# Kernel optimization log

Measured on AMD Instinct MI355X. Metric: run time of the kernel, lower is better.

## Reference

```python
import jax, jax.numpy as jnp
import numpy as np

K = 20      # kNN neighbors
H = 4       # attention heads
EPS = 1e-5  # BatchNorm eps
NEG = 0.2   # LeakyReLU negative slope


def lrelu(x):
    return jnp.where(x >= 0, x, NEG * x)


def bn(x, g, b):
    # eval-mode BatchNorm: running_mean=0, running_var=1
    return x * (g / jnp.sqrt(1.0 + EPS)) + b


def knn_idx(x):
    # x: (B, N, C) -> (B, N, K) indices of K nearest neighbors (incl. self)
    inner = -2.0 * jnp.einsum('bnc,bmc->bnm', x, x)
    xx = jnp.sum(x * x, axis=-1)
    pd = -xx[:, :, None] - inner - xx[:, None, :]  # negative squared distance
    return jax.lax.top_k(pd, K)[1]


def edge_conv(x, w, g, b):
    # EdgeConv: gather kNN features, cat(nbr-ctr, ctr), 1x1 conv, BN, LeakyReLU, max over K
    idx = knn_idx(x)                                   # (B,N,K)
    nbr = jax.vmap(lambda f, i: f[i])(x, idx)          # (B,N,K,C)
    ctr = jnp.broadcast_to(x[:, :, None, :], nbr.shape)
    e = jnp.concatenate([nbr - ctr, ctr], axis=-1)     # (B,N,K,2C)
    h = lrelu(bn(jnp.einsum('bnkc,oc->bnko', e, w), g, b))
    return jnp.max(h, axis=2)                          # (B,N,Cout)


def mha(x, w_in, b_in, w_out, b_out):
    # Faithful to source: (B,N,E) fed to nn.MultiheadAttention with batch_first=False,
    # so seq length L=B and batch=N (attention mixes across the batch axis).
    L, Nb, E = x.shape
    d = E // H
    qkv = x @ w_in.T + b_in
    q, k, v = jnp.split(qkv, 3, axis=-1)
    q = q.reshape(L, Nb, H, d) * (1.0 / np.sqrt(d))
    k = k.reshape(L, Nb, H, d)
    v = v.reshape(L, Nb, H, d)
    a = jax.nn.softmax(jnp.einsum('lnhd,mnhd->nhlm', q, k), axis=-1)
    o = jnp.einsum('nhlm,mnhd->lnhd', a, v).reshape(L, Nb, E)
    return o @ w_out.T + b_out


def setup_inputs():
    ks = iter(jax.random.split(jax.random.key(0), 64))
    def rn(shape, s=0.05):
        return jax.random.normal(next(ks), shape, jnp.float32) * s
    def gamma(c):
        return 1.0 + rn((c,), 0.1)
    B, N = 8, 1024
    inp = {'x': rn((B, N, 3), 1.0)}
    for i, (ci, co) in enumerate([(6, 64), (128, 64), (128, 128), (256, 256)], 1):
        inp[f'w{i}'] = rn((co, ci)); inp[f'g{i}'] = gamma(co); inp[f'b{i}'] = rn((co,))
    for i, e in enumerate([64, 64, 128, 256], 1):
        inp[f'a{i}_wi'] = rn((3 * e, e)); inp[f'a{i}_bi'] = rn((3 * e,))
        inp[f'a{i}_wo'] = rn((e, e));     inp[f'a{i}_bo'] = rn((e,))
    inp['w5'] = rn((1024, 512)); inp['g5'] = gamma(1024); inp['b5'] = rn((1024,))
    inp['l1w'] = rn((512, 2048)); inp['g6'] = gamma(512); inp['b6'] = rn((512,))
    inp['l2w'] = rn((256, 512)); inp['l2b'] = rn((256,))
    inp['g7'] = gamma(256); inp['b7'] = rn((256,))
    inp['l3w'] = rn((40, 256)); inp['l3b'] = rn((40,))
    return inp


def reference(x, w1, g1, b1, a1_wi, a1_bi, a1_wo, a1_bo,
              w2, g2, b2, a2_wi, a2_bi, a2_wo, a2_bo,
              w3, g3, b3, a3_wi, a3_bi, a3_wo, a3_bo,
              w4, g4, b4, a4_wi, a4_bi, a4_wo, a4_bo,
              w5, g5, b5, l1w, g6, b6, l2w, l2b, g7, b7, l3w, l3b):
    x1 = edge_conv(x, w1, g1, b1)
    x1 = mha(x1, a1_wi, a1_bi, a1_wo, a1_bo) + x1
    x2 = edge_conv(x1, w2, g2, b2)
    x2 = mha(x2, a2_wi, a2_bi, a2_wo, a2_bo) + x2
    x3 = edge_conv(x2, w3, g3, b3)
    x3 = mha(x3, a3_wi, a3_bi, a3_wo, a3_bo) + x3
    x4 = edge_conv(x3, w4, g4, b4)
    x4 = mha(x4, a4_wi, a4_bi, a4_wo, a4_bo) + x4
    h = lrelu(bn(jnp.concatenate([x1, x2, x3, x4], axis=-1) @ w5.T, g5, b5))  # (B,N,1024)
    feat = jnp.concatenate([jnp.max(h, axis=1), jnp.mean(h, axis=1)], axis=-1)  # (B,2048)
    h = lrelu(bn(feat @ l1w.T, g6, b6))
    h = lrelu(bn(h @ l2w.T + l2b, g7, b7))  # dropout is eval-mode identity
    return h @ l3w.T + l3b  # (B, 40)
```

## Files before the change

### kernel.cpp

```cpp
#include <hip/hip_runtime.h>
#include <hip/hip_bf16.h>

#define B_ 8
#define N_ 1024
#define K_ 20
#define BN_ (B_*N_)

#define BN_SCALE 0.9999950000374997f

typedef __attribute__((ext_vector_type(8))) short short8;
typedef __attribute__((ext_vector_type(4))) float f32x4;

__device__ __forceinline__ float US2F(unsigned short u) {
    union { unsigned u; float f; } c; c.u = ((unsigned)u) << 16; return c.f;
}
__device__ __forceinline__ unsigned short F2BF(float f) {
    union { float f; unsigned u; } c; c.f = f;
    unsigned r = c.u + 0x7FFF + ((c.u >> 16) & 1);
    return (unsigned short)(r >> 16);
}

__device__ __forceinline__ void ldsld16(const unsigned short* g, unsigned short* l) {
    __builtin_amdgcn_global_load_lds(
        (const __attribute__((address_space(1))) void*)g,
        (__attribute__((address_space(3))) void*)l, 16, 0, 0);
}

struct DetP { const unsigned short* g[7]; };
__device__ __forceinline__ int det_isbf(const DetP& dp) {
    int cnt = 0;
    #pragma unroll
    for (int i = 0; i < 7; i++) {
        float v = US2F(dp.g[i][0]);
        if (v > 0.5f && v < 1.5f) cnt++;
    }
    return cnt >= 4;
}

struct TPar { const void* src; void* dst; int O, I, blk0, mode; };
struct TList { TPar p[44]; };
struct TrP { const void* src; float* dst; int O, I, bx, blk0; };

__global__ __launch_bounds__(256) void k_prep(TList tl, int nent,
                                              TrP q0, TrP q1, TrP q2,
                                              int nbp, int nbtr,
                                              const void* x0, DetP dp,
                                              unsigned short* __restrict__ xa,
                                              unsigned short* __restrict__ xb,
                                              float* __restrict__ xx1) {
    __shared__ int sbf;
    if (threadIdx.x == 0) sbf = det_isbf(dp);
    __syncthreads();
    const int isbf = sbf;
    auto ld0 = [&](int idx) {
        return isbf ? US2F(((const unsigned short*)x0)[idx])
                    : ((const float*)x0)[idx];
    };
    const int bid = blockIdx.x;
    if (bid >= nbp + nbtr) {
        int blk = bid - nbp - nbtr;
        if (blk >= (BN_ * 32) / 256) {
            int i = (blk - (BN_ * 32) / 256) * 256 + threadIdx.x;
            if (i >= BN_) return;
            float s = 0.f;
            #pragma unroll
            for (int c = 0; c < 3; c++) { float v = ld0(i * 3 + c); s += v * v; }
            xx1[i] = s;
            return;
        }
        const int e = blk * 256 + threadIdx.x;
        const int i = e >> 5, p = e & 31;
        unsigned short va = 0, vb = 0;
        if (p < 9) {
            const int seg = p / 3, c = p - seg * 3;
            const float v = ld0(i * 3 + c);
            const unsigned short h = F2BF(v);
            const unsigned short l = F2BF(v - US2F(h));
            va = (seg == 1) ? l : h;
            vb = (seg < 2) ? h : l;
        }
        xa[e] = va; xb[e] = vb;
        return;
    }
    if (bid >= nbp) {
        int blk = bid - nbp;
        TrP p = q0;
        if (blk >= q2.blk0) p = q2; else if (blk >= q1.blk0) p = q1;
        blk -= p.blk0;
        const int tx = threadIdx.x & 31, ty = threadIdx.x >> 5;
        const int bi = blk % p.bx, bo = blk / p.bx;
        const int i0 = bi * 32, o0 = bo * 32;
        __shared__ float s[32][33];
        #pragma unroll
        for (int r = 0; r < 4; r++) {
            const int o = o0 + ty + r * 8, i = i0 + tx;
            if (o < p.O && i < p.I) {
                const size_t e = (size_t)o * p.I + i;
                s[ty + r * 8][tx] = isbf ? US2F(((const unsigned short*)p.src)[e])
                                         : ((const float*)p.src)[e];
            }
        }
        __syncthreads();
        #pragma unroll
        for (int r = 0; r < 4; r++) {
            const int i = i0 + ty + r * 8, o = o0 + tx;
            if (i < p.I && o < p.O) p.dst[(size_t)i * p.O + o] = s[tx][ty + r * 8];
        }
        return;
    }
    int blk = bid;
    int wi = 0;
    for (int j = nent - 1; j >= 0; j--) { if (blk >= tl.p[j].blk0) { wi = j; break; } }
    const TPar p = tl.p[wi];
    int e = (blk - p.blk0) * 256 + threadIdx.x;
    int n = p.O * p.I;
    if (e >= n) return;
    if (p.mode == 4) { ((float*)p.dst)[e] = 0.f; return; }
    int o = e / p.I, i = e - o * p.I;
    float v = isbf ? US2F(((const unsigned short*)p.src)[e])
                   : ((const float*)p.src)[e];
    if (p.mode == 0) {
        ((float*)p.dst)[(size_t)i * p.O + o] = v;
    } else if (p.mode == 2) {
        ((unsigned short*)p.dst)[e] = F2BF(v);
    } else {
        const int C = p.I >> 1;
        if (i < C) ((unsigned short*)p.dst)[(size_t)o * C + i] = F2BF(v);
        else       ((unsigned short*)p.dst)[(size_t)(p.O + o) * C + (i - C)] = F2BF(v);
    }
}

template<int KP, int TM, int TN>
__device__ __forceinline__ void pdm_dev(int bid,
                                        const unsigned short* __restrict__ xa,
                                        const unsigned short* __restrict__ xb,
                                        const float* __restrict__ xx,
                                        float* __restrict__ pd) {
    const int b = bid & 7;
    const int tt = bid >> 3;
    const int rb = (tt >> 3) * TM, cb = (tt & 7) * TN;
    const unsigned short* Ab = xa + (size_t)b * N_ * KP;
    const unsigned short* Bb = xb + (size_t)b * N_ * KP;
    const float* xxb = xx + (size_t)b * N_;
    const int t = threadIdx.x;
    __shared__ __align__(16) unsigned short As[2][TM * 32];
    __shared__ __align__(16) unsigned short Bs[2][TN * 32];
    const int w = t >> 6, lane = t & 63;
    constexpr int QR = TM / 2, QC = TN / 2;
    constexpr int MR = QR / 16, NR = QC / 16;
    const int wr = (w & 1) * QR, wc = (w >> 1) * QC;
    const int fr = lane & 15, q = lane >> 4;
    f32x4 acc[MR][NR] = {};

    auto STAGE = [&](int buf, int k0) {
        constexpr int AT = TM * 4;
        #pragma unroll
        for (int R = 0; R < (AT + 255) / 256; R++) {
            const int G = t + R * 256;
            if (AT >= (R + 1) * 256 || G < AT) {
                const int m = G >> 2, gs = (G & 3) ^ ((m >> 1) & 3);
                ldsld16(&Ab[(size_t)(rb + m) * KP + k0 + gs * 8], &As[buf][w * 512 + R * 2048]);
            }
        }
        constexpr int BT = TN * 4;
        #pragma unroll
        for (int R = 0; R < (BT + 255) / 256; R++) {
            const int G = t + R * 256;
            if (BT >= (R + 1) * 256 || G < BT) {
                const int n = G >> 2, gs = (G & 3) ^ ((n >> 1) & 3);
                ldsld16(&Bb[(size_t)(cb + n) * KP + k0 + gs * 8], &Bs[buf][w * 512 + R * 2048]);
            }
        }
    };

    constexpr int NT = KP / 32;
    STAGE(0, 0);
    asm volatile("s_waitcnt vmcnt(0)" ::: "memory");
    __builtin_amdgcn_s_barrier();
    int cur = 0;
    for (int ts = 0; ts < NT; ++ts) {
        if (ts + 1 < NT) STAGE(cur ^ 1, (ts + 1) * 32);
        short8 af[MR], bfr[NR];
        #pragma unroll
        for (int mi = 0; mi < MR; mi++) {
            const int r = wr + mi * 16 + fr;
            af[mi] = *reinterpret_cast<const short8*>(&As[cur][r * 32 + ((q ^ ((r >> 1) & 3)) << 3)]);
        }
        #pragma unroll
        for (int ni = 0; ni < NR; ni++) {
            const int r = wc + ni * 16 + fr;
            bfr[ni] = *reinterpret_cast<const short8*>(&Bs[cur][r * 32 + ((q ^ ((r >> 1) & 3)) << 3)]);
        }
        #pragma unroll
        for (int mi = 0; mi < MR; mi++) {
            #pragma unroll
            for (int ni = 0; ni < NR; ni++)
                acc[mi][ni] = __builtin_amdgcn_mfma_f32_16x16x32_bf16(af[mi], bfr[ni], acc[mi][ni], 0, 0, 0);
        }
        asm volatile("s_waitcnt vmcnt(0)" ::: "memory");
        __builtin_amdgcn_s_barrier();
        cur ^= 1;
    }
    float* pdb = pd + (size_t)b * N_ * N_;
    const int cr = (lane >> 4) * 4, cc = lane & 15;
    #pragma unroll
    for (int mi = 0; mi < MR; mi++) {
        #pragma unroll
        for (int ni = 0; ni < NR; ni++) {
            #pragma unroll
            for (int r = 0; r < 4; r++) {
                const int row = rb + wr + mi * 16 + cr + r;
                const int col = cb + wc + ni * 16 + cc;
                pdb[(size_t)row * N_ + col] = 2.f * acc[mi][ni][r] - xxb[col];
            }
        }
    }
}

template<int KD, int NC, int TM, int TN, bool CATA, bool POOL, int SPLIT>
__device__ __forceinline__ void gemm_dev(int bx, int by,
                                         const unsigned short* __restrict__ A,
                                         const unsigned short* __restrict__ A2,
                                         const unsigned short* __restrict__ A3,
                                         const unsigned short* __restrict__ A4,
                                         const unsigned short* __restrict__ Bw,
                                         const float* __restrict__ bias,
                                         const float* __restrict__ resid,
                                         float* __restrict__ Cout,
                                         float* __restrict__ Cz, int yco,
                                         int scale_cols, float qs,
                                         const float* __restrict__ gamma,
                                         const float* __restrict__ beta,
                                         unsigned short* __restrict__ obf,
                                         unsigned* __restrict__ pmaxu,
                                         float* __restrict__ psum,
                                         unsigned short* __restrict__ sxa,
                                         unsigned short* __restrict__ sxb,
                                         float* __restrict__ xxo) {
    const int t = threadIdx.x;
    const int rb = bx * TM, cb = by * TN;
    const int w = t >> 6, lane = t & 63;
    constexpr int QR = TM / 2, QC = TN / 2;
    constexpr int MR = QR / 16, NR = QC / 16;
    const int wr = (w & 1) * QR, wc = (w >> 1) * QC;
    const int fr = lane & 15, q = lane >> 4, fq = q * 8;
    f32x4 acc[MR][NR] = {};
    if constexpr (KD % 32 == 0) {
        __shared__ __align__(16) unsigned short As[2][TM * 32];
        __shared__ __align__(16) unsigned short Bs[2][TN * 32];
        auto STAGE = [&](int buf, int k0) {
            const unsigned short* Asrc = A; int AC = KD, ac0 = k0;
            if constexpr (CATA) {
                if (k0 >= 256)      { Asrc = A4; AC = 256; ac0 = k0 - 256; }
                else if (k0 >= 128) { Asrc = A3; AC = 128; ac0 = k0 - 128; }
                else if (k0 >= 64)  { Asrc = A2; AC = 64;  ac0 = k0 - 64; }
                else                { Asrc = A;  AC = 64;  ac0 = k0; }
            }
            constexpr int AT = TM * 4;
            #pragma unroll
            for (int R = 0; R < (AT + 255) / 256; R++) {
                const int G = t + R * 256;
                if (AT >= (R + 1) * 256 || G < AT) {
                    const int m = G >> 2, gs = (G & 3) ^ ((m >> 1) & 3);
                    ldsld16(&Asrc[(size_t)(rb + m) * AC + ac0 + gs * 8], &As[buf][w * 512 + R * 2048]);
                }
            }
            constexpr int BT = TN * 4;
            #pragma unroll
            for (int R = 0; R < (BT + 255) / 256; R++) {
                const int G = t + R * 256;
                if (BT >= (R + 1) * 256 || G < BT) {
                    const int n = G >> 2, gs = (G & 3) ^ ((n >> 1) & 3);
                    ldsld16(&Bw[(size_t)(cb + n) * KD + k0 + gs * 8], &Bs[buf][w * 512 + R * 2048]);
                }
            }
        };
        constexpr int NT = KD / 32;
        STAGE(0, 0);
        asm volatile("s_waitcnt vmcnt(0)" ::: "memory");
        __builtin_amdgcn_s_barrier();
        int cur = 0;
        for (int ts = 0; ts < NT; ++ts) {
            if (ts + 1 < NT) STAGE(cur ^ 1, (ts + 1) * 32);
            short8 af[MR], bfr[NR];
            #pragma unroll
            for (int mi = 0; mi < MR; mi++) {
                const int r = wr + mi * 16 + fr;
                af[mi] = *reinterpret_cast<const short8*>(&As[cur][r * 32 + ((q ^ ((r >> 1) & 3)) << 3)]);
            }
            #pragma unroll
            for (int ni = 0; ni < NR; ni++) {
                const int r = wc + ni * 16 + fr;
                bfr[ni] = *reinterpret_cast<const short8*>(&Bs[cur][r * 32 + ((q ^ ((r >> 1) & 3)) << 3)]);
            }
            #pragma unroll
            for (int mi = 0; mi < MR; mi++) {
                #pragma unroll
                for (int ni = 0; ni < NR; ni++)
                    acc[mi][ni] = __builtin_amdgcn_mfma_f32_16x16x32_bf16(af[mi], bfr[ni], acc[mi][ni], 0, 0, 0);
            }
            asm volatile("s_waitcnt vmcnt(0)" ::: "memory");
            __builtin_amdgcn_s_barrier();
            cur ^= 1;
        }
    } else {
        __shared__ __align__(16) unsigned short As[TM * 40];
        __shared__ __align__(16) unsigned short Bs[TN * 40];
        for (int k0 = 0; k0 < KD; k0 += 32) {
            __syncthreads();
            #pragma unroll
            for (int u = t; u < TM * 4; u += 256) {
                const int m = u >> 2, c = (u & 3) * 8;
                #pragma unroll
                for (int j = 0; j < 8; j++) {
                    const int kk = k0 + c + j;
                    As[m * 40 + c + j] = (kk < KD) ? A[(size_t)(rb + m) * KD + kk] : (unsigned short)0;
                }
            }
            #pragma unroll
            for (int u = t; u < TN * 4; u += 256) {
                const int n = u >> 2, c = (u & 3) * 8;
                const int gn = cb + n;
                if (gn < NC) {
                    #pragma unroll
                    for (int j = 0; j < 8; j++) {
                        const int kk = k0 + c + j;
                        Bs[n * 40 + c + j] = (kk < KD) ? Bw[(size_t)gn * KD + kk] : (unsigned short)0;
                    }
                } else {
                    short8 z = {};
                    *reinterpret_cast<short8*>(&Bs[n * 40 + c]) = z;
                }
            }
            __syncthreads();
            short8 af[MR], bfr[NR];
            #pragma unroll
            for (int mi = 0; mi < MR; mi++)
                af[mi] = *reinterpret_cast<const short8*>(&As[(wr + mi * 16 + fr) * 40 + fq]);
            #pragma unroll
            for (int ni = 0; ni < NR; ni++)
                bfr[ni] = *reinterpret_cast<const short8*>(&Bs[(wc + ni * 16 + fr) * 40 + fq]);
            #pragma unroll
            for (int mi = 0; mi < MR; mi++) {
                #pragma unroll
                for (int ni = 0; ni < NR; ni++)
                    acc[mi][ni] = __builtin_amdgcn_mfma_f32_16x16x32_bf16(af[mi], bfr[ni], acc[mi][ni], 0, 0, 0);
            }
        }
    }
    const int cr = (lane >> 4) * 4, cc = lane & 15;
    if constexpr (POOL) {
        const int bidx = rb >> 10;
        #pragma unroll
        for (int ni = 0; ni < NR; ni++) {
            const int col = cb + wc + ni * 16 + cc;
            const float gm = gamma[col] * BN_SCALE, bt = beta[col];
            float sm = 0.f, mxv = -3e38f;
            #pragma unroll
            for (int mi = 0; mi < MR; mi++) {
                #pragma unroll
                for (int r = 0; r < 4; r++) {
                    float v = acc[mi][ni][r] * gm + bt;
                    v = v >= 0.f ? v : 0.2f * v;
                    sm += v; mxv = fmaxf(mxv, v);
                }
            }
            sm += __shfl_xor(sm, 16, 64);
            sm += __shfl_xor(sm, 32, 64);
            mxv = fmaxf(mxv, __shfl_xor(mxv, 16, 64));
            mxv = fmaxf(mxv, __shfl_xor(mxv, 32, 64));
            if (lane < 16) {
                atomicAdd(&psum[bidx * 1024 + col], sm);
                unsigned tb = __float_as_uint(mxv);
                tb = (tb & 0x80000000u) ? ~tb : (tb | 0x80000000u);
                atomicMax(&pmaxu[bidx * 1024 + col], tb);
            }
        }
    } else {
        float sx[MR][4] = {};
        #pragma unroll
        for (int mi = 0; mi < MR; mi++) {
            #pragma unroll
            for (int ni = 0; ni < NR; ni++) {
                #pragma unroll
                for (int r = 0; r < 4; r++) {
                    const int row = rb + wr + mi * 16 + cr + r;
                    const int col = cb + wc + ni * 16 + cc;
                    if (col < NC) {
                        float v = acc[mi][ni][r] + (bias ? bias[col] : 0.f);
                        if (col < scale_cols) v *= qs;
                        if (resid) v += resid[(size_t)row * NC + col];
                        if (gamma) {
                            v = v * (gamma[col] * BN_SCALE) + beta[col];
                            v = v >= 0.f ? v : 0.2f * v;
                        }
                        if (yco > 0) {
                            if (col < yco) Cout[(size_t)row * yco + col] = v;
                            else           Cz[(size_t)row * yco + (col - yco)] = v;
                        } else {
                            Cout[(size_t)row * NC + col] = v;
                        }
                        if (obf) obf[(size_t)row * NC + col] = F2BF(v);
                        if constexpr (SPLIT > 0) {
                            constexpr int KP2 = 3 * SPLIT;
                            const unsigned short h = F2BF(v);
                            const unsigned short l = F2BF(v - US2F(h));
                            sxa[(size_t)row * KP2 + 0 * SPLIT + col] = h;
                            sxa[(size_t)row * KP2 + 1 * SPLIT + col] = l;
                            sxa[(size_t)row * KP2 + 2 * SPLIT + col] = h;
                            sxb[(size_t)row * KP2 + 0 * SPLIT + col] = h;
                            sxb[(size_t)row * KP2 + 1 * SPLIT + col] = h;
                            sxb[(size_t)row * KP2 + 2 * SPLIT + col] = l;
                            sx[mi][r] += v * v;
                        }
                    }
                }
            }
        }
        if constexpr (SPLIT > 0) {
            #pragma unroll
            for (int mi = 0; mi < MR; mi++) {
                #pragma unroll
                for (int r = 0; r < 4; r++) {
                    float s = sx[mi][r];
                    s += __shfl_xor(s, 1, 64);
                    s += __shfl_xor(s, 2, 64);
                    s += __shfl_xor(s, 4, 64);
                    s += __shfl_xor(s, 8, 64);
                    if ((lane & 15) == 0)
                        atomicAdd(&xxo[rb + wr + mi * 16 + cr + r], s);
                }
            }
        }
    }
}

template<int KD, int NC, int TM, int TN, bool CATA = false, bool POOL = false, int SPLIT = 0, bool AFF = false>
__global__ __launch_bounds__(256) void k_gemmb(const unsigned short* __restrict__ A,
                                               const unsigned short* __restrict__ A2,
                                               const unsigned short* __restrict__ A3,
                                               const unsigned short* __restrict__ A4,
                                               const unsigned short* __restrict__ Bw,
                                               const float* __restrict__ bias,
                                               const float* __restrict__ resid,
                                               float* __restrict__ Cout,
                                               int scale_cols, float qs,
                                               const float* __restrict__ gamma,
                                               const float* __restrict__ beta,
                                               unsigned short* __restrict__ obf,
                                               unsigned* __restrict__ pmaxu,
                                               float* __restrict__ psum,
                                               unsigned short* __restrict__ sxa,
                                               unsigned short* __restrict__ sxb,
                                               float* __restrict__ xxo) {
    int bx = blockIdx.x;
    if constexpr (AFF) bx = (bx & 7) * (gridDim.x >> 3) + (bx >> 3);
    gemm_dev<KD, NC, TM, TN, CATA, POOL, SPLIT>(bx, blockIdx.y,
        A, A2, A3, A4, Bw, bias, resid, Cout, nullptr, 0, scale_cols, qs, gamma, beta,
        obf, pmaxu, psum, sxa, sxb, xxo);
}

template<int KP, int KDY, int NCY, int TMY, int TNY>
__global__ __launch_bounds__(256) void k_pdmyz(const unsigned short* __restrict__ xa,
                                               const unsigned short* __restrict__ xb,
                                               const float* __restrict__ xx,
                                               float* __restrict__ pd,
                                               const unsigned short* __restrict__ Ay,
                                               const unsigned short* __restrict__ Bwy,
                                               float* __restrict__ Cy,
                                               float* __restrict__ Cz, int yco, int gxy) {
    if ((int)blockIdx.x < 512) { pdm_dev<KP, 128, 128>(blockIdx.x, xa, xb, xx, pd); return; }
    const int g = blockIdx.x - 512;
    const int batch = g & 7, rem = g >> 3;
    const int rpb = gxy >> 3;
    const int bx = batch * rpb + rem % rpb;
    const int by = rem / rpb;
    gemm_dev<KDY, NCY, TMY, TNY, false, false, 0>(bx, by,
        Ay, nullptr, nullptr, nullptr, Bwy, nullptr, nullptr, Cy, Cz, yco, 0, 1.f,
        nullptr, nullptr, nullptr, nullptr, nullptr, nullptr, nullptr, nullptr);
}

template<int CO>
__global__ __launch_bounds__(256) void k_seledge(const float* __restrict__ pd,
                                                 const float* __restrict__ y,
                                                 const float* __restrict__ z,
                                                 const float* __restrict__ g,
                                                 const float* __restrict__ bb,
                                                 float* __restrict__ out,
                                                 unsigned short* __restrict__ outb) {
    const int t = threadIdx.x;
    const int w = t >> 6, lane = t & 63;
    const int blk = blockIdx.x;
    const int b = blk & 7;
    const int i0 = (b << 10) + ((blk >> 3) << 2);
    const int bbase = b << 10;
    __shared__ int sidx[4][K_];
    {
        const int i = i0 + w;
        const float* row = pd + (size_t)b * N_ * N_ + (size_t)(i & 1023) * N_;
        unsigned key[16];
        #pragma unroll
        for (int q = 0; q < 16; q++) {
            const int j = q * 64 + lane;
            unsigned bits = __float_as_uint(row[j]);
            bits = (bits & 0x80000000u) ? ~bits : (bits | 0x80000000u);
            key[q] = (bits & 0xFFFFFC00u) | (unsigned)(N_ - 1 - j);
        }
        int myj = 0;
        for (int kk = 0; kk < K_; kk++) {
            unsigned m = key[0];
            #pragma unroll
            for (int u = 1; u < 16; u++) m = key[u] > m ? key[u] : m;
            #pragma unroll
            for (int s = 1; s < 64; s <<= 1) {
                unsigned o = (unsigned)__shfl_xor((int)m, s, 64);
                m = o > m ? o : m;
            }
            const int j = N_ - 1 - (int)(m & 1023u);
            if (lane == kk) myj = j;
            #pragma unroll
            for (int u = 0; u < 16; u++)
                if (key[u] == m) key[u] = 0u;
        }
        if (lane < K_) sidx[w][lane] = myj;
    }
    __syncthreads();
    constexpr int TPP = CO / 4;
    if (t < 4 * TPP) {
        const int p = t / TPP;
        const int cw = (t % TPP) * 4;
        const int ig = i0 + p;
        float4 m = {-3e38f, -3e38f, -3e38f, -3e38f};
        #pragma unroll 4
        for (int k = 0; k < K_; k++) {
            const int jg = bbase + sidx[p][k];
            const float4 yv = *reinterpret_cast<const float4*>(&y[(size_t)jg * CO + cw]);
            m.x = fmaxf(m.x, yv.x); m.y = fmaxf(m.y, yv.y);
            m.z = fmaxf(m.z, yv.z); m.w = fmaxf(m.w, yv.w);
        }
        const float4 yi = *reinterpret_cast<const float4*>(&y[(size_t)ig * CO + cw]);
        const float4 zi = *reinterpret_cast<const float4*>(&z[(size_t)ig * CO + cw]);
        const float4 gv = *reinterpret_cast<const float4*>(&g[cw]);
        const float4 bv = *reinterpret_cast<const float4*>(&bb[cw]);
        float vals[4] = {m.x - yi.x + zi.x, m.y - yi.y + zi.y,
                         m.z - yi.z + zi.z, m.w - yi.w + zi.w};
        float gs[4] = {gv.x, gv.y, gv.z, gv.w};
        float bs[4] = {bv.x, bv.y, bv.z, bv.w};
        float4 o;
        float* op = &o.x;
        #pragma unroll
        for (int j = 0; j < 4; j++) {
            float h = vals[j] * (gs[j] * BN_SCALE) + bs[j];
            op[j] = h >= 0.f ? h : 0.2f * h;
        }
        *reinterpret_cast<float4*>(&out[(size_t)ig * CO + cw]) = o;
        #pragma unroll
        for (int j = 0; j < 4; j++) outb[(size_t)ig * CO + cw + j] = F2BF(op[j]);
    }
}

template<int E, int SPLIT>
__global__ __launch_bounds__(256) void k_attnout(const float* __restrict__ qkv,
                                                 const unsigned short* __restrict__ wo,
                                                 const float* __restrict__ bo,
                                                 float* __restrict__ x,
                                                 unsigned short* __restrict__ xob,
                                                 unsigned short* __restrict__ sxa,
                                                 unsigned short* __restrict__ sxb,
                                                 float* __restrict__ xxo) {
    constexpr int H = 4, D = E / H, L = 8;
    const int n = blockIdx.x;
    const int t = threadIdx.x;
    const int h = t >> 6, lane = t & 63;
    __shared__ float sq[L][3 * E];
    __shared__ float so[L][E];
    __shared__ unsigned short swo[E][E + 8];
    __shared__ float sxx[L];
    for (int u = t; u < L * 3 * E; u += 256) {
        int l = u / (3 * E), r = u - l * (3 * E);
        sq[l][r] = qkv[(size_t)(l * N_ + n) * (3 * E) + r];
    }
    for (int u = t; u < E * E; u += 256) swo[u / E][u % E] = wo[u];
    if (t < L) sxx[t] = 0.f;
    __syncthreads();
    const int l = lane >> 3, m = lane & 7;
    float s = 0.f;
    #pragma unroll 8
    for (int dd = 0; dd < D; dd++)
        s += sq[l][h * D + dd] * sq[m][E + h * D + dd];
    float mx = s;
    #pragma unroll
    for (int st = 1; st < 8; st <<= 1) mx = fmaxf(mx, __shfl_xor(mx, st, 64));
    float e = expf(s - mx);
    float sum = e;
    #pragma unroll
    for (int st = 1; st < 8; st <<= 1) sum += __shfl_xor(sum, st, 64);
    const float p = e / sum;
    float pm[8];
    #pragma unroll
    for (int mm = 0; mm < 8; mm++) pm[mm] = __shfl(p, (lane & 56) | mm, 64);
    #pragma unroll
    for (int j = 0; j < D / 8; j++) {
        const int dd = m + 8 * j;
        float a = 0.f;
        #pragma unroll
        for (int mm = 0; mm < 8; mm++) a += pm[mm] * sq[mm][2 * E + h * D + dd];
        so[l][h * D + dd] = a;
    }
    __syncthreads();
    for (int u = t; u < L * E; u += 256)
        so[u / E][u % E] = US2F(F2BF(so[u / E][u % E]));
    __syncthreads();
    constexpr int PT = (L * E) / 256;
    #pragma unroll
    for (int it = 0; it < PT; it++) {
        const int item = t + it * 256;
        const int ll = item / E, ee = item % E;
        float acc = 0.f;
        #pragma unroll 16
        for (int c = 0; c < E; c++)
            acc += so[ll][c] * US2F(swo[ee][c]);
        const int row = ll * N_ + n;
        const float v = acc + bo[ee] + x[(size_t)row * E + ee];
        x[(size_t)row * E + ee] = v;
        xob[(size_t)row * E + ee] = F2BF(v);
        if constexpr (SPLIT > 0) {
            constexpr int KP2 = 3 * SPLIT;
            const unsigned short hh = F2BF(v);
            const unsigned short lo = F2BF(v - US2F(hh));
            sxa[(size_t)row * KP2 + 0 * SPLIT + ee] = hh;
            sxa[(size_t)row * KP2 + 1 * SPLIT + ee] = lo;
            sxa[(size_t)row * KP2 + 2 * SPLIT + ee] = hh;
            sxb[(size_t)row * KP2 + 0 * SPLIT + ee] = hh;
            sxb[(size_t)row * KP2 + 1 * SPLIT + ee] = hh;
            sxb[(size_t)row * KP2 + 2 * SPLIT + ee] = lo;
            float vs = v * v;
            #pragma unroll
            for (int st = 1; st < 64; st <<= 1) vs += __shfl_xor(vs, st, 64);
            if (lane == 0) atomicAdd(&sxx[ll], vs);
        }
    }
    if constexpr (SPLIT > 0) {
        __syncthreads();
        if (t < L) xxo[t * N_ + n] = sxx[t];
    }
}

__global__ __launch_bounds__(256) void k_attnout4(const float* __restrict__ qkv,
                                                  const unsigned short* __restrict__ wo,
                                                  const float* __restrict__ bo,
                                                  float* __restrict__ x,
                                                  unsigned short* __restrict__ xob) {
    constexpr int E = 256, H = 4, D = E / H, L = 8;
    const int n = blockIdx.x;
    const int t = threadIdx.x;
    const int h = t >> 6, lane = t & 63;
    __shared__ float sq[L][3 * E];
    __shared__ float so[L][E];
    __shared__ float swoc[E][33];
    for (int u = t; u < L * 3 * E; u += 256) {
        int l = u / (3 * E), r = u - l * (3 * E);
        sq[l][r] = qkv[(size_t)(l * N_ + n) * (3 * E) + r];
    }
    __syncthreads();
    const int l = lane >> 3, m = lane & 7;
    float s = 0.f;
    #pragma unroll 8
    for (int dd = 0; dd < D; dd++)
        s += sq[l][h * D + dd] * sq[m][E + h * D + dd];
    float mx = s;
    #pragma unroll
    for (int st = 1; st < 8; st <<= 1) mx = fmaxf(mx, __shfl_xor(mx, st, 64));
    float e = expf(s - mx);
    float sum = e;
    #pragma unroll
    for (int st = 1; st < 8; st <<= 1) sum += __shfl_xor(sum, st, 64);
    const float p = e / sum;
    float pm[8];
    #pragma unroll
    for (int mm = 0; mm < 8; mm++) pm[mm] = __shfl(p, (lane & 56) | mm, 64);
    #pragma unroll
    for (int j = 0; j < D / 8; j++) {
        const int dd = m + 8 * j;
        float a = 0.f;
        #pragma unroll
        for (int mm = 0; mm < 8; mm++) a += pm[mm] * sq[mm][2 * E + h * D + dd];
        so[l][h * D + dd] = a;
    }
    __syncthreads();
    for (int u = t; u < L * E; u += 256)
        so[u / E][u % E] = US2F(F2BF(so[u / E][u % E]));
    constexpr int PT = (L * E) / 256;
    float acc[PT] = {};
    for (int ch = 0; ch < 8; ch++) {
        __syncthreads();
        for (int u = t; u < E * 32; u += 256) {
            const int ee = u >> 5, cc = u & 31;
            swoc[ee][cc] = US2F(wo[ee * E + ch * 32 + cc]);
        }
        __syncthreads();
        #pragma unroll
        for (int it = 0; it < PT; it++) {
            const int item = t + it * 256;
            const int ll = item / E, ee = item % E;
            float a = acc[it];
            #pragma unroll
            for (int cc = 0; cc < 32; cc++)
                a += so[ll][ch * 32 + cc] * swoc[ee][cc];
            acc[it] = a;
        }
    }
    #pragma unroll
    for (int it = 0; it < PT; it++) {
        const int item = t + it * 256;
        const int ll = item / E, ee = item % E;
        const int row = ll * N_ + n;
        const float v = acc[it] + bo[ee] + x[(size_t)row * E + ee];
        x[(size_t)row * E + ee] = v;
        xob[(size_t)row * E + ee] = F2BF(v);
    }
}

__global__ __launch_bounds__(256) void k_fc1(const unsigned* __restrict__ pmaxu,
                                             const float* __restrict__ psum,
                                             const float* __restrict__ l1wT,
                                             const float* __restrict__ g6, const float* __restrict__ b6,
                                             float* __restrict__ f1) {
    int oc = blockIdx.x, b = blockIdx.y, t = threadIdx.x;
    __shared__ float fin[2048];
    __shared__ float ps[4][64];
    for (int u = t; u < 2048; u += 256) {
        float v;
        if (u < 1024) {
            unsigned tb = pmaxu[b * 1024 + u];
            unsigned bits = (tb & 0x80000000u) ? (tb & 0x7FFFFFFFu) : ~tb;
            v = __uint_as_float(bits);
        } else {
            v = psum[b * 1024 + (u - 1024)] * (1.f / 1024.f);
        }
        fin[u] = v;
    }
    __syncthreads();
    int ol = t & 63, kc = t >> 6;
    int o = oc * 64 + ol;
    float acc = 0.f;
    for (int c = kc * 512; c < kc * 512 + 512; c++) acc += fin[c] * l1wT[(size_t)c * 512 + o];
    ps[kc][ol] = acc;
    __syncthreads();
    if (t < 64) {
        int oo = oc * 64 + t;
        float a = ps[0][t] + ps[1][t] + ps[2][t] + ps[3][t];
        float h = a * (g6[oo] * BN_SCALE) + b6[oo];
        f1[b * 512 + oo] = h >= 0.f ? h : 0.2f * h;
    }
}

__global__ __launch_bounds__(256) void k_fc23(const float* __restrict__ f1, const float* __restrict__ l2wT,
                                              const float* __restrict__ l2b,
                                              const float* __restrict__ g7, const float* __restrict__ b7,
                                              const float* __restrict__ l3wT, const float* __restrict__ l3b,
                                              void* __restrict__ out, DetP dp) {
    int b = blockIdx.x, t = threadIdx.x;
    __shared__ float fin[512];
    __shared__ float f2s[256];
    __shared__ int sbf;
    if (t == 0) sbf = det_isbf(dp);
    for (int u = t; u < 512; u += 256) fin[u] = f1[b * 512 + u];
    __syncthreads();
    {
        float acc = 0.f;
        for (int c = 0; c < 512; c++) acc += fin[c] * l2wT[(size_t)c * 256 + t];
        acc += l2b[t];
        float h = acc * (g7[t] * BN_SCALE) + b7[t];
        f2s[t] = h >= 0.f ? h : 0.2f * h;
    }
    __syncthreads();
    if (t < 40) {
        float acc = 0.f;
        for (int c = 0; c < 256; c++) acc += f2s[c] * l3wT[(size_t)c * 40 + t];
        acc += l3b[t];
        if (sbf) ((__hip_bfloat16*)out)[b * 40 + t] = __float2bfloat16(acc);
        else     ((float*)out)[b * 40 + t] = acc;
    }
}

extern "C" void kernel_launch(void* const* d_in, const int* in_sizes, int n_in,
                              void* d_out, int out_size, void* d_ws, size_t ws_size,
                              hipStream_t stream) {
    auto us = [&](int i) { return (const unsigned short*)d_in[i]; };

    float* ws = (float*)d_ws;
    size_t off = 0;
    auto A = [&](size_t n) { float* p = ws + off; off += (n + 3) & ~(size_t)3; return p; };
    auto AU = [&](size_t n) { return (unsigned short*)A((n + 1) / 2); };
    float* x1   = A((size_t)BN_ * 64);
    float* x2   = A((size_t)BN_ * 64);
    float* x3   = A((size_t)BN_ * 128);
    float* x4   = A((size_t)BN_ * 256);
    float* pd   = A((size_t)BN_ * 1024);
    float* f1   = A(8 * 512);
    float* xx   = A(4 * BN_);
    float* qkvw = A((size_t)BN_ * 768);
    unsigned short* xa = AU((size_t)BN_ * 384);
    unsigned short* xb = AU((size_t)BN_ * 384);
    unsigned short* xf0b = AU((size_t)BN_ * 3);
    unsigned short* x1b  = AU((size_t)BN_ * 64);
    unsigned short* x2b  = AU((size_t)BN_ * 64);
    unsigned short* x3b  = AU((size_t)BN_ * 128);
    unsigned short* x4b  = AU((size_t)BN_ * 256);
    unsigned* pmaxu = (unsigned*)A(8 * 1024);
    float*    psum  = A(8 * 1024);
    unsigned short* w1yzb = AU(128 * 3);
    unsigned short* w2yzb = AU(128 * 64);
    unsigned short* w3yzb = AU(256 * 64);
    unsigned short* w4yzb = AU(512 * 128);
    unsigned short* a1wib = AU(192 * 64);  unsigned short* a1wob = AU(64 * 64);
    unsigned short* a2wib = AU(192 * 64);  unsigned short* a2wob = AU(64 * 64);
    unsigned short* a3wib = AU(384 * 128); unsigned short* a3wob = AU(128 * 128);
    unsigned short* a4wib = AU(768 * 256); unsigned short* a4wob = AU(256 * 256);
    unsigned short* w5b   = AU(1024 * 512);
    float* l1wT  = A(2048 * 512);
    float* l2wT  = A(512 * 256);
    float* l3wT  = A(256 * 40);
    float* g1f = A(64);   float* b1f = A(64);
    float* g2f = A(64);   float* b2f = A(64);
    float* g3f = A(128);  float* b3f = A(128);
    float* g4f = A(256);  float* b4f = A(256);
    float* bi1 = A(192);  float* bo1 = A(64);
    float* bi2 = A(192);  float* bo2 = A(64);
    float* bi3 = A(384);  float* bo3 = A(128);
    float* bi4 = A(768);  float* bo4 = A(256);
    float* g5f = A(1024); float* b5f = A(1024);
    float* g6f = A(512);  float* b6f = A(512);
    float* l2bf = A(256);
    float* g7f = A(256);  float* b7f = A(256);
    float* l3bf = A(40);

    float* xx1 = xx;              float* xx2 = xx + BN_;
    float* xx3 = xx + 2 * BN_;    float* xx4 = xx + 3 * BN_;

    float* yy = qkvw;
    float* zz = qkvw + (size_t)BN_ * 256;

    DetP dp{{us(2), us(5), us(8), us(11), us(30), us(33), us(37)}};

    TList tl; int nb = 0; int k = 0;
    auto add = [&](int i, void* dst, int O, int I, int mode) {
        tl.p[k].src = d_in[i]; tl.p[k].dst = dst; tl.p[k].O = O; tl.p[k].I = I;
        tl.p[k].blk0 = nb; tl.p[k].mode = mode;
        nb += (O * I + 255) / 256; k++;
    };
    add(0,  xf0b,  BN_ * 3, 1, 2);
    add(0,  pmaxu, 16384, 1, 4);
    add(1,  w1yzb, 64, 6, 3);
    add(4,  w2yzb, 64, 128, 3);
    add(7,  w3yzb, 128, 128, 3);
    add(10, w4yzb, 256, 256, 3);
    add(13, a1wib, 192, 64, 2);
    add(15, a1wob, 64, 64, 2);
    add(17, a2wib, 192, 64, 2);
    add(19, a2wob, 64, 64, 2);
    add(21, a3wib, 384, 128, 2);
    add(23, a3wob, 128, 128, 2);
    add(25, a4wib, 768, 256, 2);
    add(27, a4wob, 256, 256, 2);
    add(29, w5b,   1024, 512, 2);
    add(2,  g1f, 64, 1, 0);   add(3,  b1f, 64, 1, 0);
    add(5,  g2f, 64, 1, 0);   add(6,  b2f, 64, 1, 0);
    add(8,  g3f, 128, 1, 0);  add(9,  b3f, 128, 1, 0);
    add(11, g4f, 256, 1, 0);  add(12, b4f, 256, 1, 0);
    add(14, bi1, 192, 1, 0);  add(16, bo1, 64, 1, 0);
    add(18, bi2, 192, 1, 0);  add(20, bo2, 64, 1, 0);
    add(22, bi3, 384, 1, 0);  add(24, bo3, 128, 1, 0);
    add(26, bi4, 768, 1, 0);  add(28, bo4, 256, 1, 0);
    add(30, g5f, 1024, 1, 0); add(31, b5f, 1024, 1, 0);
    add(33, g6f, 512, 1, 0);  add(34, b6f, 512, 1, 0);
    add(36, l2bf, 256, 1, 0);
    add(37, g7f, 256, 1, 0);  add(38, b7f, 256, 1, 0);
    add(40, l3bf, 40, 1, 0);

    TrP tp1{d_in[32], l1wT, 512, 2048, 2048 / 32, 0};
    TrP tp2{d_in[35], l2wT, 256, 512,  512 / 32,  (2048 / 32) * (512 / 32)};
    TrP tp3{d_in[39], l3wT, 40,  256,  256 / 32,  tp2.blk0 + (512 / 32) * (256 / 32)};
    const int trblocks = tp3.blk0 + (256 / 32) * ((40 + 31) / 32);
    const int splblocks = (BN_ * 32) / 256 + 32;
    k_prep<<<nb + trblocks + splblocks, 256, 0, stream>>>(
        tl, k, tp1, tp2, tp3, nb, trblocks, d_in[0], dp, xa, xb, xx1);

    const unsigned short* N0 = nullptr;
    unsigned short* U0 = nullptr;
    unsigned* NU = nullptr; float* NF = nullptr;

    k_pdmyz<32, 3, 128, 64, 64><<<512 + 256, 256, 0, stream>>>(xa, xb, xx1, pd, xf0b, w1yzb, yy, zz, 64, 128);
    k_seledge<64><<<2048, 256, 0, stream>>>(pd, yy, zz, g1f, b1f, x1, x1b);
    k_gemmb<64, 192, 64, 64, false, false, 0, true><<<dim3(128, 3), 256, 0, stream>>>(x1b, N0, N0, N0, a1wib, bi1, nullptr, qkvw, 64, 0.25f, nullptr, nullptr, nullptr, NU, NF, U0, U0, NF);
    k_attnout<64, 64><<<N_, 256, 0, stream>>>(qkvw, a1wob, bo1, x1, x1b, xa, xb, xx2);

    k_pdmyz<192, 64, 128, 64, 64><<<512 + 256, 256, 0, stream>>>(xa, xb, xx2, pd, x1b, w2yzb, yy, zz, 64, 128);
    k_seledge<64><<<2048, 256, 0, stream>>>(pd, yy, zz, g2f, b2f, x2, x2b);
    k_gemmb<64, 192, 64, 64, false, false, 0, true><<<dim3(128, 3), 256, 0, stream>>>(x2b, N0, N0, N0, a2wib, bi2, nullptr, qkvw, 64, 0.25f, nullptr, nullptr, nullptr, NU, NF, U0, U0, NF);
    k_attnout<64, 64><<<N_, 256, 0, stream>>>(qkvw, a2wob, bo2, x2, x2b, xa, xb, xx3);

    k_pdmyz<192, 64, 256, 64, 64><<<512 + 512, 256, 0, stream>>>(xa, xb, xx3, pd, x2b, w3yzb, yy, zz, 128, 128);
    k_seledge<128><<<2048, 256, 0, stream>>>(pd, yy, zz, g3f, b3f, x3, x3b);
    k_gemmb<128, 384, 64, 128, false, false, 0, true><<<dim3(128, 3), 256, 0, stream>>>(x3b, N0, N0, N0, a3wib, bi3, nullptr, qkvw, 128, 0.17677669529663687f, nullptr, nullptr, nullptr, NU, NF, U0, U0, NF);
    k_attnout<128, 128><<<N_, 256, 0, stream>>>(qkvw, a3wob, bo3, x3, x3b, xa, xb, xx4);

    k_pdmyz<384, 128, 512, 128, 128><<<512 + 256, 256, 0, stream>>>(xa, xb, xx4, pd, x3b, w4yzb, yy, zz, 256, 64);
    k_seledge<256><<<2048, 256, 0, stream>>>(pd, yy, zz, g4f, b4f, x4, x4b);
    k_gemmb<256, 768, 64, 128, false, false, 0, true><<<dim3(128, 6), 256, 0, stream>>>(x4b, N0, N0, N0, a4wib, bi4, nullptr, qkvw, 256, 0.125f, nullptr, nullptr, nullptr, NU, NF, U0, U0, NF);
    k_attnout4<<<N_, 256, 0, stream>>>(qkvw, a4wob, bo4, x4, x4b);

    k_gemmb<512, 1024, 128, 128, true, true, 0, true><<<dim3(64, 8), 256, 0, stream>>>(
        x1b, x2b, x3b, x4b, w5b, nullptr, nullptr, nullptr, 0, 1.f, g5f, b5f, nullptr, pmaxu, psum, U0, U0, NF);
    k_fc1<<<dim3(8, 8), 256, 0, stream>>>(pmaxu, psum, l1wT, g6f, b6f, f1);
    k_fc23<<<8, 256, 0, stream>>>(f1, l2wT, l2bf, g7f, b7f, l3wT, l3bf, d_out, dp);
}
```

Before: 520.0 us.

## Split layer-4 attention output projection into separate MFMA GEMM

Replaces the fused layer-4 attention+output-projection kernel, which did the 256x256 out-projection with scalar FP32 FMAs per point, with two stages. An attention-only kernel writes bf16 head outputs to a new buffer, and the existing bf16 matrix-core GEMM then applies the projection, bias and residual add. This moves the heaviest scalar arithmetic onto matrix cores, at the cost of an extra launch and a global round trip of the attention output.

```diff
diff --git a/kernel.cpp b/kernel.cpp
--- a/kernel.cpp
+++ b/kernel.cpp
@@ -559,6 +559,51 @@
     }
 }
 
+template<int E>
+__global__ __launch_bounds__(256) void k_attn(const float* __restrict__ qkv,
+                                              unsigned short* __restrict__ o) {
+    constexpr int H = 4, D = E / H, L = 8;
+    const int n = blockIdx.x;
+    const int t = threadIdx.x;
+    const int h = t >> 6, lane = t & 63;
+    __shared__ float sq[L][3 * E];
+    __shared__ float so[L][E];
+    for (int u = t; u < L * 3 * E; u += 256) {
+        int l = u / (3 * E), r = u - l * (3 * E);
+        sq[l][r] = qkv[(size_t)(l * N_ + n) * (3 * E) + r];
+    }
+    __syncthreads();
+    const int l = lane >> 3, m = lane & 7;
+    float s = 0.f;
+    #pragma unroll 8
+    for (int dd = 0; dd < D; dd++)
+        s += sq[l][h * D + dd] * sq[m][E + h * D + dd];
+    float mx = s;
+    #pragma unroll
+    for (int st = 1; st < 8; st <<= 1) mx = fmaxf(mx, __shfl_xor(mx, st, 64));
+    float e = expf(s - mx);
+    float sum = e;
+    #pragma unroll
+    for (int st = 1; st < 8; st <<= 1) sum += __shfl_xor(sum, st, 64);
+    const float p = e / sum;
+    float pm[8];
+    #pragma unroll
+    for (int mm = 0; mm < 8; mm++) pm[mm] = __shfl(p, (lane & 56) | mm, 64);
+    #pragma unroll
+    for (int j = 0; j < D / 8; j++) {
+        const int dd = m + 8 * j;
+        float a = 0.f;
+        #pragma unroll
+        for (int mm = 0; mm < 8; mm++) a += pm[mm] * sq[mm][2 * E + h * D + dd];
+        so[l][h * D + dd] = a;
+    }
+    __syncthreads();
+    for (int u = t; u < L * E; u += 256) {
+        int l2 = u / E, e2 = u - l2 * E;
+        o[(size_t)(l2 * N_ + n) * E + e2] = F2BF(so[l2][e2]);
+    }
+}
+
 template<int E, int SPLIT>
 __global__ __launch_bounds__(256) void k_attnout(const float* __restrict__ qkv,
                                                  const unsigned short* __restrict__ wo,
@@ -646,81 +691,6 @@
     }
 }
 
-__global__ __launch_bounds__(256) void k_attnout4(const float* __restrict__ qkv,
-                                                  const unsigned short* __restrict__ wo,
-                                                  const float* __restrict__ bo,
-                                                  float* __restrict__ x,
-                                                  unsigned short* __restrict__ xob) {
-    constexpr int E = 256, H = 4, D = E / H, L = 8;
-    const int n = blockIdx.x;
-    const int t = threadIdx.x;
-    const int h = t >> 6, lane = t & 63;
-    __shared__ float sq[L][3 * E];
-    __shared__ float so[L][E];
-    __shared__ float swoc[E][33];
-    for (int u = t; u < L * 3 * E; u += 256) {
-        int l = u / (3 * E), r = u - l * (3 * E);
-        sq[l][r] = qkv[(size_t)(l * N_ + n) * (3 * E) + r];
-    }
-    __syncthreads();
-    const int l = lane >> 3, m = lane & 7;
-    float s = 0.f;
-    #pragma unroll 8
-    for (int dd = 0; dd < D; dd++)
-        s += sq[l][h * D + dd] * sq[m][E + h * D + dd];
-    float mx = s;
-    #pragma unroll
-    for (int st = 1; st < 8; st <<= 1) mx = fmaxf(mx, __shfl_xor(mx, st, 64));
-    float e = expf(s - mx);
-    float sum = e;
-    #pragma unroll
-    for (int st = 1; st < 8; st <<= 1) sum += __shfl_xor(sum, st, 64);
-    const float p = e / sum;
-    float pm[8];
-    #pragma unroll
-    for (int mm = 0; mm < 8; mm++) pm[mm] = __shfl(p, (lane & 56) | mm, 64);
-    #pragma unroll
-    for (int j = 0; j < D / 8; j++) {
-        const int dd = m + 8 * j;
-        float a = 0.f;
-        #pragma unroll
-        for (int mm = 0; mm < 8; mm++) a += pm[mm] * sq[mm][2 * E + h * D + dd];
-        so[l][h * D + dd] = a;
-    }
-    __syncthreads();
-    for (int u = t; u < L * E; u += 256)
-        so[u / E][u % E] = US2F(F2BF(so[u / E][u % E]));
-    constexpr int PT = (L * E) / 256;
-    float acc[PT] = {};
-    for (int ch = 0; ch < 8; ch++) {
-        __syncthreads();
-        for (int u = t; u < E * 32; u += 256) {
-            const int ee = u >> 5, cc = u & 31;
-            swoc[ee][cc] = US2F(wo[ee * E + ch * 32 + cc]);
-        }
-        __syncthreads();
-        #pragma unroll
-        for (int it = 0; it < PT; it++) {
-            const int item = t + it * 256;
-            const int ll = item / E, ee = item % E;
-            float a = acc[it];
-            #pragma unroll
-            for (int cc = 0; cc < 32; cc++)
-                a += so[ll][ch * 32 + cc] * swoc[ee][cc];
-            acc[it] = a;
-        }
-    }
-    #pragma unroll
-    for (int it = 0; it < PT; it++) {
-        const int item = t + it * 256;
-        const int ll = item / E, ee = item % E;
-        const int row = ll * N_ + n;
-        const float v = acc[it] + bo[ee] + x[(size_t)row * E + ee];
-        x[(size_t)row * E + ee] = v;
-        xob[(size_t)row * E + ee] = F2BF(v);
-    }
-}
-
 __global__ __launch_bounds__(256) void k_fc1(const unsigned* __restrict__ pmaxu,
                                              const float* __restrict__ psum,
                                              const float* __restrict__ l1wT,
@@ -808,6 +778,7 @@
     unsigned short* x2b  = AU((size_t)BN_ * 64);
     unsigned short* x3b  = AU((size_t)BN_ * 128);
     unsigned short* x4b  = AU((size_t)BN_ * 256);
+    unsigned short* owb  = AU((size_t)BN_ * 256);
     unsigned* pmaxu = (unsigned*)A(8 * 1024);
     float*    psum  = A(8 * 1024);
     unsigned short* w1yzb = AU(128 * 3);
@@ -909,7 +880,8 @@
     k_pdmyz<384, 128, 512, 128, 128><<<512 + 256, 256, 0, stream>>>(xa, xb, xx4, pd, x3b, w4yzb, yy, zz, 256, 64);
     k_seledge<256><<<2048, 256, 0, stream>>>(pd, yy, zz, g4f, b4f, x4, x4b);
     k_gemmb<256, 768, 64, 128, false, false, 0, true><<<dim3(128, 6), 256, 0, stream>>>(x4b, N0, N0, N0, a4wib, bi4, nullptr, qkvw, 256, 0.125f, nullptr, nullptr, nullptr, NU, NF, U0, U0, NF);
-    k_attnout4<<<N_, 256, 0, stream>>>(qkvw, a4wob, bo4, x4, x4b);
+    k_attn<256><<<N_, 256, 0, stream>>>(qkvw, owb);
+    k_gemmb<256, 256, 64, 128, false, false, 0, true><<<dim3(128, 2), 256, 0, stream>>>(owb, N0, N0, N0, a4wob, bo4, x4, x4, 0, 1.f, nullptr, nullptr, x4b, NU, NF, U0, U0, NF);
 
     k_gemmb<512, 1024, 128, 128, true, true, 0, true><<<dim3(64, 8), 256, 0, stream>>>(
         x1b, x2b, x3b, x4b, w5b, nullptr, nullptr, nullptr, 0, 1.f, g5f, b5f, nullptr, pmaxu, psum, U0, U0, NF);
```

Result: faster. 476.0 us (-8.5%).
